# Kernel optimization log

Measured on AMD Instinct MI355X. Metric: run time of the kernel, lower is better.

Reference implementation:

```python
import jax, jax.numpy as jnp
import numpy as np

B, S, D = 2, 4096, 1024

def setup_inputs() -> dict:
    key = jax.random.key(0)
    k1, k2 = jax.random.split(key)
    x = jax.random.normal(k1, (B, S, D), dtype=jnp.float32)
    W = jax.random.normal(k2, (D, 3 * D), dtype=jnp.float32) * (1.0 / np.sqrt(D))
    b = jnp.zeros((3 * D,), dtype=jnp.float32)
    return {"x": x, "W": W, "b": b}

def reference(x, W, b) -> jnp.ndarray:
    D_ = x.shape[-1]
    qkv = x @ W + b                       # [B, S, 3D]
    q, k, v = jnp.split(qkv, 3, axis=2)    # each [B, S, D]
    scale = 1.0 / jnp.sqrt(jnp.asarray(D_, dtype=x.dtype))
    scores = jnp.einsum('bqd,bkd->bqk', q, k) * scale  # [B, S, S]
    weights = jax.nn.softmax(scores, axis=-1)
    return jnp.einsum('bqk,bkd->bqd', weights, v)       # [B, S, D]
```

## Files before the change

### kernel.cpp

```cpp
#include <hip/hip_runtime.h>
#include <hip/hip_bf16.h>

typedef __attribute__((ext_vector_type(4))) float  f32x4;
typedef __attribute__((ext_vector_type(8))) __bf16 bf16x8;
typedef __attribute__((ext_vector_type(8))) unsigned short u16x8;

typedef const __attribute__((address_space(1))) void gas_void;
typedef __attribute__((address_space(3))) void las_void;

__device__ __forceinline__ unsigned short f2bf(float x) {
    unsigned u = __builtin_bit_cast(unsigned, x);
    u += 0x7fffu + ((u >> 16) & 1u);
    return (unsigned short)(u >> 16);
}
__device__ __forceinline__ float bf2f(unsigned short h) {
    unsigned u = ((unsigned)h) << 16;
    return __builtin_bit_cast(float, u);
}
__device__ __forceinline__ void gload_lds16(const void* g, void* l) {
    __builtin_amdgcn_global_load_lds((gas_void*)g, (las_void*)l, 16, 0, 0);
}

#define WAITVM(N) asm volatile("s_waitcnt vmcnt(" #N ")" ::: "memory")
#define BAR() do { __builtin_amdgcn_s_barrier(); __builtin_amdgcn_sched_barrier(0); } while (0)

__global__ void k_f32_to_bf16(const float* __restrict__ in,
                              unsigned short* __restrict__ out, int n4) {
    int i = blockIdx.x * blockDim.x + threadIdx.x;
    if (i < n4) {
        float4 v = ((const float4*)in)[i];
        ushort4 o;
        o.x = f2bf(v.x); o.y = f2bf(v.y); o.z = f2bf(v.z); o.w = f2bf(v.w);
        ((ushort4*)out)[i] = o;
    }
}

__global__ void k_transpose_w(const float* __restrict__ W,
                              unsigned short* __restrict__ Wt,
                              int K, int N) {
    __shared__ unsigned short tile[32][33];
    int n0 = blockIdx.x * 32, k0 = blockIdx.y * 32;
    int tx = threadIdx.x, ty = threadIdx.y;
#pragma unroll
    for (int i = 0; i < 4; i++) {
        int kk = ty + i * 8;
        tile[kk][tx] = f2bf(W[(size_t)(k0 + kk) * N + n0 + tx]);
    }
    __syncthreads();
#pragma unroll
    for (int i = 0; i < 4; i++) {
        int nn = ty + i * 8;
        Wt[(size_t)(n0 + nn) * K + k0 + tx] = tile[tx][nn];
    }
}

__global__ __launch_bounds__(256, 2) void k_g128qkv(
        const unsigned short* __restrict__ A, int lda,
        const unsigned short* __restrict__ Bt, int ldb,
        unsigned short* __restrict__ C,
        unsigned short* __restrict__ Vt,
        const float* __restrict__ bias, int K) {
    __shared__ __align__(16) unsigned short As[2][8192];
    __shared__ __align__(16) unsigned short Bs[2][8192];

    const int nwg  = gridDim.x * gridDim.y;
    const int flat = blockIdx.y * gridDim.x + blockIdx.x;
    const int swzb = (flat & 7) * (nwg >> 3) + (flat >> 3);
    const int m0   = (swzb / gridDim.x) * 128;
    const int n0   = (swzb % gridDim.x) * 128;

    const int tid  = threadIdx.x;
    const int lane = tid & 63;
    const int wid  = tid >> 6;
    const int wr   = wid >> 1;
    const int wc   = wid & 1;
    const int l15  = lane & 15;
    const int l4   = lane >> 4;

    f32x4 acc[4][4] = {};

    const int srow = tid >> 3;
    const int kel  = (((lane & 7) ^ (lane >> 3)) << 3);
    const int c0 = (l4 << 4) ^ ((l15 & 7) << 4);
    const int c1 = (64 + (l4 << 4)) ^ ((l15 & 7) << 4);

    auto stA = [&](int b, int g, int kt) {
        gload_lds16(A + (size_t)(m0 + g * 32 + srow) * lda + kt * 64 + kel,
                    (char*)As + b * 16384 + g * 4096 + (wid << 10));
    };
    auto stB = [&](int b, int g, int kt) {
        gload_lds16(Bt + (size_t)(n0 + g * 32 + srow) * ldb + kt * 64 + kel,
                    (char*)Bs + b * 16384 + g * 4096 + (wid << 10));
    };

#define MM(I, J, X, Y) \
    acc[I][J] = __builtin_amdgcn_mfma_f32_16x16x32_bf16((X), (Y), acc[I][J], 0, 0, 0)

    const int NT = K >> 6;
    stA(0, 0, 0); stA(0, 1, 0); stA(0, 2, 0); stA(0, 3, 0);
    stB(0, 0, 0); stB(0, 1, 0); stB(0, 2, 0); stB(0, 3, 0);

    for (int t = 0; t < NT; t++) {
        const int cur = t & 1, nxt = cur ^ 1;
        const char* Ab = (const char*)As + cur * 16384;
        const char* Bb = (const char*)Bs + cur * 16384;
        const bool hn = (t + 1 < NT);

        bf16x8 af[4], bq[4];

        if (hn) {
            stA(nxt, 0, t + 1); stA(nxt, 1, t + 1); stA(nxt, 2, t + 1); stA(nxt, 3, t + 1);
            WAITVM(4);
        } else {
            WAITVM(0);
        }
        BAR();
#pragma unroll
        for (int mf = 0; mf < 4; mf++)
            af[mf] = *(const bf16x8*)(Ab + (wr * 64 + mf * 16 + l15) * 128 + c0);
#pragma unroll
        for (int nf = 0; nf < 4; nf++)
            bq[nf] = *(const bf16x8*)(Bb + (wc * 64 + nf * 16 + l15) * 128 + c0);
        __builtin_amdgcn_s_setprio(1);
#pragma unroll
        for (int mf = 0; mf < 4; mf++)
#pragma unroll
        for (int nf = 0; nf < 4; nf++)
            MM(mf, nf, af[mf], bq[nf]);
        __builtin_amdgcn_s_setprio(0);

        if (hn) {
            stB(nxt, 0, t + 1); stB(nxt, 1, t + 1); stB(nxt, 2, t + 1); stB(nxt, 3, t + 1);
        }
#pragma unroll
        for (int mf = 0; mf < 4; mf++)
            af[mf] = *(const bf16x8*)(Ab + (wr * 64 + mf * 16 + l15) * 128 + c1);
#pragma unroll
        for (int nf = 0; nf < 4; nf++)
            bq[nf] = *(const bf16x8*)(Bb + (wc * 64 + nf * 16 + l15) * 128 + c1);
        __builtin_amdgcn_s_setprio(1);
#pragma unroll
        for (int mf = 0; mf < 4; mf++)
#pragma unroll
        for (int nf = 0; nf < 4; nf++)
            MM(mf, nf, af[mf], bq[nf]);
        __builtin_amdgcn_s_setprio(0);
        BAR();
    }
#undef MM

#pragma unroll
    for (int mf = 0; mf < 4; mf++) {
        const int row = m0 + wr * 64 + mf * 16 + l4 * 4;
#pragma unroll
        for (int nf = 0; nf < 4; nf++) {
            const int col = n0 + wc * 64 + nf * 16 + l15;
            const f32x4 av = acc[mf][nf];
            const float bv = bias[col];
            const int lc = col & 1023;
            if (col < 2048) {
#pragma unroll
                for (int r = 0; r < 4; r++)
                    C[(size_t)(col >> 10) * 8388608 +
                      (size_t)(row + r) * 1024 + lc] = f2bf(av[r] + bv);
            } else {
                const int b = row >> 12, s = row & 4095;
                ushort4 o;
                o.x = f2bf(av[0] + bv); o.y = f2bf(av[1] + bv);
                o.z = f2bf(av[2] + bv); o.w = f2bf(av[3] + bv);
                *(ushort4*)&Vt[(size_t)b * 4194304 + (size_t)lc * 4096 + s] = o;
            }
        }
    }
}

__global__ __launch_bounds__(512, 2) void k_scores(
        const unsigned short* __restrict__ A,
        const unsigned short* __restrict__ Bt,
        unsigned short* __restrict__ C,
        float* __restrict__ part,
        int K, float scale, long sA, long sB, long sC) {
    __shared__ __align__(16) unsigned short As[2][16384];
    __shared__ __align__(16) unsigned short Bs[2][16384];

    const int z = blockIdx.z;
    A  += (size_t)z * sA;
    Bt += (size_t)z * sB;

    const int flat = blockIdx.y * gridDim.x + blockIdx.x;
    const int xcd  = flat & 7;
    const int i    = flat >> 3;
    const int m0   = (((xcd >> 1) << 2) + (i >> 3)) * 256;
    const int n0   = (((xcd & 1) << 3) + (i & 7)) * 256;

    const int tid  = threadIdx.x;
    const int lane = tid & 63;
    const int wid  = tid >> 6;
    const int wm   = wid >> 2;
    const int wn   = wid & 3;
    const int l15  = lane & 15;
    const int l4   = lane >> 4;

    f32x4 acc[8][4] = {};

    const int srow = tid >> 3;
    const int kel  = (((lane & 7) ^ (lane >> 3)) << 3);
    const int c0 = ((l4 << 4)) ^ ((l15 & 7) << 4);
    const int c1 = (64 + (l4 << 4)) ^ ((l15 & 7) << 4);

    auto stageA = [&](int b, int h, int kt) {
#pragma unroll
        for (int c = 0; c < 2; c++) {
            const int r = h * 128 + c * 64 + srow;
            gload_lds16(A + (size_t)(m0 + r) * 1024 + kt * 64 + kel,
                        (char*)As + b * 32768 + h * 16384 + c * 8192 + (wid << 10));
        }
    };
    auto stageB = [&](int b, int h, int kt) {
#pragma unroll
        for (int c = 0; c < 2; c++) {
            const int r = h * 128 + c * 64 + srow;
            gload_lds16(Bt + (size_t)(n0 + r) * 1024 + kt * 64 + kel,
                        (char*)Bs + b * 32768 + h * 16384 + c * 8192 + (wid << 10));
        }
    };

#define MM(I, J, X, Y) \
    acc[I][J] = __builtin_amdgcn_mfma_f32_16x16x32_bf16((X), (Y), acc[I][J], 0, 0, 0)

    const int NT = K >> 6;
    stageA(0, 0, 0); stageB(0, 0, 0); stageA(0, 1, 0); stageB(0, 1, 0);

    for (int t = 0; t < NT; t++) {
        const int cur = t & 1, nxt = cur ^ 1;
        const char* Ab = (const char*)As + cur * 32768;
        const char* Bb = (const char*)Bs + cur * 32768;

        if (t + 1 < NT) {
            stageA(nxt, 0, t + 1); stageB(nxt, 0, t + 1);
            stageA(nxt, 1, t + 1); stageB(nxt, 1, t + 1);
            WAITVM(8);
        } else {
            WAITVM(0);
        }
        BAR();

        bf16x8 bfrg[2][2][2];
#pragma unroll
        for (int qn = 0; qn < 2; qn++)
#pragma unroll
        for (int nf = 0; nf < 2; nf++) {
            const int rb = (wn * 64 + qn * 32 + nf * 16 + l15) * 128;
            bfrg[qn][nf][0] = *(const bf16x8*)(Bb + rb + c0);
            bfrg[qn][nf][1] = *(const bf16x8*)(Bb + rb + c1);
        }
        {
            bf16x8 af[4][2];
#pragma unroll
            for (int mf = 0; mf < 4; mf++) {
                const int ra = (wm * 128 + 0 * 64 + mf * 16 + l15) * 128;
                af[mf][0] = *(const bf16x8*)(Ab + ra + c0);
                af[mf][1] = *(const bf16x8*)(Ab + ra + c1);
            }
            __builtin_amdgcn_s_setprio(1);
#pragma unroll
            for (int mf = 0; mf < 4; mf++)
#pragma unroll
            for (int qn = 0; qn < 2; qn++)
#pragma unroll
            for (int nf = 0; nf < 2; nf++) {
                MM(mf, qn * 2 + nf, af[mf][0], bfrg[qn][nf][0]);
                MM(mf, qn * 2 + nf, af[mf][1], bfrg[qn][nf][1]);
            }
            __builtin_amdgcn_s_setprio(0);
        }

        {
            bf16x8 af[4][2];
#pragma unroll
            for (int mf = 0; mf < 4; mf++) {
                const int ra = (wm * 128 + 1 * 64 + mf * 16 + l15) * 128;
                af[mf][0] = *(const bf16x8*)(Ab + ra + c0);
                af[mf][1] = *(const bf16x8*)(Ab + ra + c1);
            }
            __builtin_amdgcn_s_setprio(1);
#pragma unroll
            for (int mf = 0; mf < 4; mf++)
#pragma unroll
            for (int qn = 0; qn < 2; qn++)
#pragma unroll
            for (int nf = 0; nf < 2; nf++) {
                MM(4 + mf, qn * 2 + nf, af[mf][0], bfrg[qn][nf][0]);
                MM(4 + mf, qn * 2 + nf, af[mf][1], bfrg[qn][nf][1]);
            }
            __builtin_amdgcn_s_setprio(0);
        }
        __builtin_amdgcn_s_barrier();
        __builtin_amdgcn_sched_barrier(0);
    }
#undef MM

    const int cb4 = ((n0 >> 8) << 2) + wn;
#pragma unroll
    for (int qm = 0; qm < 2; qm++)
#pragma unroll
    for (int mf = 0; mf < 4; mf++) {
        const int row = m0 + wm * 128 + qm * 64 + mf * 16 + l4 * 4;
        float rs[4] = {0.f, 0.f, 0.f, 0.f};
#pragma unroll
        for (int qn = 0; qn < 2; qn++)
#pragma unroll
        for (int nf = 0; nf < 2; nf++) {
            const int col = n0 + wn * 64 + qn * 32 + nf * 16 + l15;
            const f32x4 av = acc[qm * 4 + mf][qn * 2 + nf];
#pragma unroll
            for (int r = 0; r < 4; r++) {
                const float e = __expf(av[r] * scale);
                rs[r] += e;
                C[(size_t)z * sC + (size_t)(row + r) * 4096 + col] = f2bf(e);
            }
        }
#pragma unroll
        for (int r = 0; r < 4; r++) {
#pragma unroll
            for (int o = 1; o < 16; o <<= 1)
                rs[r] += __shfl_xor(rs[r], o);
        }
        if (l15 == 0) {
#pragma unroll
            for (int r = 0; r < 4; r++)
                part[((size_t)z * 4096 + row + r) * 64 + cb4] = rs[r];
        }
    }
}

__global__ __launch_bounds__(256) void k_rinv(const float* __restrict__ part,
                                              float* __restrict__ rinv, int nrows) {
    int row = blockIdx.x * blockDim.x + threadIdx.x;
    if (row < nrows) {
        const float* p = part + (size_t)row * 64;
        float s = 0.f;
#pragma unroll
        for (int i = 0; i < 16; i++) {
            f32x4 v = *(const f32x4*)(p + i * 4);
            s += v[0] + v[1] + v[2] + v[3];
        }
        rinv[row] = 1.0f / s;
    }
}

__global__ __launch_bounds__(512, 2) void k_pv256(
        const unsigned short* __restrict__ A,
        const unsigned short* __restrict__ Bt,
        float* __restrict__ C,
        const float* __restrict__ rinv,
        int K, long sA, long sB, long sC) {
    __shared__ __align__(16) unsigned short As[3][16384];
    __shared__ __align__(16) unsigned short Bs[3][8192];

    const int z = blockIdx.z;
    A  += (size_t)z * sA;
    Bt += (size_t)z * sB;

    const int nwg  = gridDim.x * gridDim.y;
    const int flat = blockIdx.y * gridDim.x + blockIdx.x;
    const int swzb = (flat & 7) * (nwg >> 3) + (flat >> 3);
    const int m0   = (swzb / gridDim.x) * 256;
    const int n0   = (swzb % gridDim.x) * 128;

    const int tid  = threadIdx.x;
    const int lane = tid & 63;
    const int wid  = tid >> 6;
    const int wm   = wid >> 2;
    const int wn   = wid & 3;
    const int l15  = lane & 15;
    const int l4   = lane >> 4;

    f32x4 acc[8][2] = {};

    const int srow = tid >> 3;
    const int kel  = (((lane & 7) ^ (lane >> 3)) << 3);
    const int c0 = ((l4 << 4)) ^ ((l15 & 7) << 4);
    const int c1 = (64 + (l4 << 4)) ^ ((l15 & 7) << 4);

    auto stageA1 = [&](int b, int a, int kt) {
        const int r = a * 64 + srow;
        gload_lds16(A + (size_t)(m0 + r) * 4096 + kt * 64 + kel,
                    (char*)As + b * 32768 + a * 8192 + (wid << 10));
    };
    auto stageB1 = [&](int b, int c, int kt) {
        const int r = c * 64 + srow;
        gload_lds16(Bt + (size_t)(n0 + r) * 4096 + kt * 64 + kel,
                    (char*)Bs + b * 16384 + c * 8192 + (wid << 10));
    };
    auto stageTile = [&](int b, int kt) {
        stageA1(b, 0, kt); stageA1(b, 1, kt);
        stageA1(b, 2, kt); stageA1(b, 3, kt);
        stageB1(b, 0, kt); stageB1(b, 1, kt);
    };

#define MM(I, J, X, Y) \
    acc[I][J] = __builtin_amdgcn_mfma_f32_16x16x32_bf16((X), (Y), acc[I][J], 0, 0, 0)

    const int NT = K >> 6;
    stageTile(0, 0);
    stageTile(1, 1);

    for (int t = 0; t < NT; t++) {
        const int cur = t % 3;
        const char* Ab = (const char*)As + cur * 32768;
        const char* Bb = (const char*)Bs + cur * 16384;

        if (t + 2 < NT) {
            stageTile((t + 2) % 3, t + 2);
            WAITVM(12);
        } else if (t + 1 < NT) {
            WAITVM(6);
        } else {
            WAITVM(0);
        }
        BAR();

        bf16x8 bfrg[2][2];
#pragma unroll
        for (int nf = 0; nf < 2; nf++) {
            const int rb = (wn * 32 + nf * 16 + l15) * 128;
            bfrg[nf][0] = *(const bf16x8*)(Bb + rb + c0);
            bfrg[nf][1] = *(const bf16x8*)(Bb + rb + c1);
        }
        {
            bf16x8 af[4][2];
#pragma unroll
            for (int mf = 0; mf < 4; mf++) {
                const int ra = (wm * 128 + 0 * 64 + mf * 16 + l15) * 128;
                af[mf][0] = *(const bf16x8*)(Ab + ra + c0);
                af[mf][1] = *(const bf16x8*)(Ab + ra + c1);
            }
            __builtin_amdgcn_s_setprio(1);
#pragma unroll
            for (int mf = 0; mf < 4; mf++)
#pragma unroll
            for (int nf = 0; nf < 2; nf++) {
                MM(mf, nf, af[mf][0], bfrg[nf][0]);
                MM(mf, nf, af[mf][1], bfrg[nf][1]);
            }
            __builtin_amdgcn_s_setprio(0);
        }

        {
            bf16x8 af[4][2];
#pragma unroll
            for (int mf = 0; mf < 4; mf++) {
                const int ra = (wm * 128 + 1 * 64 + mf * 16 + l15) * 128;
                af[mf][0] = *(const bf16x8*)(Ab + ra + c0);
                af[mf][1] = *(const bf16x8*)(Ab + ra + c1);
            }
            __builtin_amdgcn_s_setprio(1);
#pragma unroll
            for (int mf = 0; mf < 4; mf++)
#pragma unroll
            for (int nf = 0; nf < 2; nf++) {
                MM(4 + mf, nf, af[mf][0], bfrg[nf][0]);
                MM(4 + mf, nf, af[mf][1], bfrg[nf][1]);
            }
            __builtin_amdgcn_s_setprio(0);
        }
        __builtin_amdgcn_s_barrier();
        __builtin_amdgcn_sched_barrier(0);
    }
#undef MM

#pragma unroll
    for (int qm = 0; qm < 2; qm++)
#pragma unroll
    for (int mf = 0; mf < 4; mf++) {
        const int row = m0 + wm * 128 + qm * 64 + mf * 16 + l4 * 4;
        const f32x4 riv = *(const f32x4*)&rinv[(size_t)z * 4096 + row];
#pragma unroll
        for (int nf = 0; nf < 2; nf++) {
            const int col = n0 + wn * 32 + nf * 16 + l15;
            const f32x4 av = acc[qm * 4 + mf][nf];
#pragma unroll
            for (int r = 0; r < 4; r++)
                C[(size_t)z * sC + (size_t)(row + r) * 1024 + col] = av[r] * riv[r];
        }
    }
}

extern "C" void kernel_launch(void* const* d_in, const int* in_sizes, int n_in,
                              void* d_out, int out_size, void* d_ws, size_t ws_size,
                              hipStream_t stream) {
    const float* x    = (const float*)d_in[0];
    const float* W    = (const float*)d_in[1];
    const float* bias = (const float*)d_in[2];
    float* out        = (float*)d_out;

    char* ws = (char*)d_ws;
    unsigned short* Qb   = (unsigned short*)(ws);
    unsigned short* Vt   = (unsigned short*)(ws + 33554432);
    unsigned short* xb   = (unsigned short*)(ws + 50331648);
    unsigned short* Wt   = (unsigned short*)(ws + 67108864);
    unsigned short* Pcat = (unsigned short*)(ws + 50331648);
    float*          part = (float*)(ws + 117440512);
    float*          rinv = (float*)(ws + 121634816);

    k_f32_to_bf16<<<8192, 256, 0, stream>>>(x, xb, (8192 * 1024) / 4);
    k_transpose_w<<<dim3(96, 32), dim3(32, 8), 0, stream>>>(W, Wt, 1024, 3072);
    k_g128qkv<<<dim3(24, 64), 256, 0, stream>>>(xb, 1024, Wt, 1024, Qb, Vt, bias, 1024);

    const float scale = 0.03125f;
    k_scores<<<dim3(16, 16, 2), 512, 0, stream>>>(
        Qb, Qb + 8388608, Pcat, part, 1024, scale, 4194304, 4194304, 16777216);
    k_rinv<<<32, 256, 0, stream>>>(part, rinv, 8192);
    k_pv256<<<dim3(8, 16, 2), 512, 0, stream>>>(
        Pcat, Vt, out, rinv, 4096, 16777216, 4194304, 4194304);
}
```

Before: 258.8 us.

## Replace 256x256 scores GEMM with 128x128 tiles and split A/B staging

Swaps the scores kernel from 256x256 tiles with 512 threads and K-step 64 for 128x128 tiles with 256 threads and K-step 32, launching 2048 blocks instead of 512. The grid gets an XCD-aware swizzle, the LDS swizzle is adjusted, and B-tile prefetch moves after the MFMA block so A and B loads are spread across the iteration. The aim is better occupancy and load balance on the 256 CUs, at the cost of less operand reuse per tile, more global traffic, and more barriers per unit of work. Partial row sums still fit in 64 slots per row.

```diff
diff --git a/kernel.cpp b/kernel.cpp
--- a/kernel.cpp
+++ b/kernel.cpp
@@ -174,145 +174,97 @@
     }
 }
 
-__global__ __launch_bounds__(512, 2) void k_scores(
+__global__ __launch_bounds__(256, 2) void k_s128(
         const unsigned short* __restrict__ A,
         const unsigned short* __restrict__ Bt,
         unsigned short* __restrict__ C,
         float* __restrict__ part,
         int K, float scale, long sA, long sB, long sC) {
-    __shared__ __align__(16) unsigned short As[2][16384];
-    __shared__ __align__(16) unsigned short Bs[2][16384];
+    __shared__ __align__(16) unsigned short As[2][4096];
+    __shared__ __align__(16) unsigned short Bs[2][4096];
 
     const int z = blockIdx.z;
     A  += (size_t)z * sA;
     Bt += (size_t)z * sB;
 
+    const int nwg  = gridDim.x * gridDim.y;
     const int flat = blockIdx.y * gridDim.x + blockIdx.x;
-    const int xcd  = flat & 7;
-    const int i    = flat >> 3;
-    const int m0   = (((xcd >> 1) << 2) + (i >> 3)) * 256;
-    const int n0   = (((xcd & 1) << 3) + (i & 7)) * 256;
+    const int swzb = (flat & 7) * (nwg >> 3) + (flat >> 3);
+    const int m0   = (swzb / gridDim.x) * 128;
+    const int n0   = (swzb % gridDim.x) * 128;
 
     const int tid  = threadIdx.x;
     const int lane = tid & 63;
     const int wid  = tid >> 6;
-    const int wm   = wid >> 2;
-    const int wn   = wid & 3;
+    const int wr   = wid >> 1;
+    const int wc   = wid & 1;
     const int l15  = lane & 15;
     const int l4   = lane >> 4;
 
-    f32x4 acc[8][4] = {};
-
-    const int srow = tid >> 3;
-    const int kel  = (((lane & 7) ^ (lane >> 3)) << 3);
-    const int c0 = ((l4 << 4)) ^ ((l15 & 7) << 4);
-    const int c1 = (64 + (l4 << 4)) ^ ((l15 & 7) << 4);
-
-    auto stageA = [&](int b, int h, int kt) {
-#pragma unroll
-        for (int c = 0; c < 2; c++) {
-            const int r = h * 128 + c * 64 + srow;
-            gload_lds16(A + (size_t)(m0 + r) * 1024 + kt * 64 + kel,
-                        (char*)As + b * 32768 + h * 16384 + c * 8192 + (wid << 10));
-        }
-    };
-    auto stageB = [&](int b, int h, int kt) {
-#pragma unroll
-        for (int c = 0; c < 2; c++) {
-            const int r = h * 128 + c * 64 + srow;
-            gload_lds16(Bt + (size_t)(n0 + r) * 1024 + kt * 64 + kel,
-                        (char*)Bs + b * 32768 + h * 16384 + c * 8192 + (wid << 10));
-        }
+    f32x4 acc[4][4] = {};
+
+    const int srow = tid >> 2;
+    const int kel  = (((tid & 3) ^ ((tid >> 2) & 3)) << 3);
+    const int csw  = ((l4 ^ (l15 & 3)) << 4);
+
+    auto stA = [&](int b, int g, int kt) {
+        gload_lds16(A + (size_t)(m0 + g * 64 + srow) * 1024 + kt * 32 + kel,
+                    (char*)As + b * 8192 + g * 4096 + (wid << 10));
+    };
+    auto stB = [&](int b, int g, int kt) {
+        gload_lds16(Bt + (size_t)(n0 + g * 64 + srow) * 1024 + kt * 32 + kel,
+                    (char*)Bs + b * 8192 + g * 4096 + (wid << 10));
     };
 
 #define MM(I, J, X, Y) \
     acc[I][J] = __builtin_amdgcn_mfma_f32_16x16x32_bf16((X), (Y), acc[I][J], 0, 0, 0)
 
-    const int NT = K >> 6;
-    stageA(0, 0, 0); stageB(0, 0, 0); stageA(0, 1, 0); stageB(0, 1, 0);
+    const int NT = K >> 5;
+    stA(0, 0, 0); stA(0, 1, 0); stB(0, 0, 0); stB(0, 1, 0);
 
     for (int t = 0; t < NT; t++) {
         const int cur = t & 1, nxt = cur ^ 1;
-        const char* Ab = (const char*)As + cur * 32768;
-        const char* Bb = (const char*)Bs + cur * 32768;
-
-        if (t + 1 < NT) {
-            stageA(nxt, 0, t + 1); stageB(nxt, 0, t + 1);
-            stageA(nxt, 1, t + 1); stageB(nxt, 1, t + 1);
-            WAITVM(8);
+        const char* Ab = (const char*)As + cur * 8192;
+        const char* Bb = (const char*)Bs + cur * 8192;
+        const bool hn = (t + 1 < NT);
+
+        if (hn) {
+            stA(nxt, 0, t + 1); stA(nxt, 1, t + 1);
+            WAITVM(2);
         } else {
             WAITVM(0);
         }
         BAR();
 
-        bf16x8 bfrg[2][2][2];
-#pragma unroll
-        for (int qn = 0; qn < 2; qn++)
-#pragma unroll
-        for (int nf = 0; nf < 2; nf++) {
-            const int rb = (wn * 64 + qn * 32 + nf * 16 + l15) * 128;
-            bfrg[qn][nf][0] = *(const bf16x8*)(Bb + rb + c0);
-            bfrg[qn][nf][1] = *(const bf16x8*)(Bb + rb + c1);
-        }
-        {
-            bf16x8 af[4][2];
-#pragma unroll
-            for (int mf = 0; mf < 4; mf++) {
-                const int ra = (wm * 128 + 0 * 64 + mf * 16 + l15) * 128;
-                af[mf][0] = *(const bf16x8*)(Ab + ra + c0);
-                af[mf][1] = *(const bf16x8*)(Ab + ra + c1);
-            }
-            __builtin_amdgcn_s_setprio(1);
-#pragma unroll
-            for (int mf = 0; mf < 4; mf++)
-#pragma unroll
-            for (int qn = 0; qn < 2; qn++)
-#pragma unroll
-            for (int nf = 0; nf < 2; nf++) {
-                MM(mf, qn * 2 + nf, af[mf][0], bfrg[qn][nf][0]);
-                MM(mf, qn * 2 + nf, af[mf][1], bfrg[qn][nf][1]);
-            }
-            __builtin_amdgcn_s_setprio(0);
-        }
-
-        {
-            bf16x8 af[4][2];
-#pragma unroll
-            for (int mf = 0; mf < 4; mf++) {
-                const int ra = (wm * 128 + 1 * 64 + mf * 16 + l15) * 128;
-                af[mf][0] = *(const bf16x8*)(Ab + ra + c0);
-                af[mf][1] = *(const bf16x8*)(Ab + ra + c1);
-            }
-            __builtin_amdgcn_s_setprio(1);
-#pragma unroll
-            for (int mf = 0; mf < 4; mf++)
-#pragma unroll
-            for (int qn = 0; qn < 2; qn++)
-#pragma unroll
-            for (int nf = 0; nf < 2; nf++) {
-                MM(4 + mf, qn * 2 + nf, af[mf][0], bfrg[qn][nf][0]);
-                MM(4 + mf, qn * 2 + nf, af[mf][1], bfrg[qn][nf][1]);
-            }
-            __builtin_amdgcn_s_setprio(0);
-        }
-        __builtin_amdgcn_s_barrier();
-        __builtin_amdgcn_sched_barrier(0);
+        bf16x8 af[4], bq[4];
+#pragma unroll
+        for (int mf = 0; mf < 4; mf++)
+            af[mf] = *(const bf16x8*)(Ab + (wr * 64 + mf * 16 + l15) * 64 + csw);
+#pragma unroll
+        for (int nf = 0; nf < 4; nf++)
+            bq[nf] = *(const bf16x8*)(Bb + (wc * 64 + nf * 16 + l15) * 64 + csw);
+        __builtin_amdgcn_s_setprio(1);
+#pragma unroll
+        for (int mf = 0; mf < 4; mf++)
+#pragma unroll
+        for (int nf = 0; nf < 4; nf++)
+            MM(mf, nf, af[mf], bq[nf]);
+        __builtin_amdgcn_s_setprio(0);
+
+        if (hn) { stB(nxt, 0, t + 1); stB(nxt, 1, t + 1); }
+        BAR();
     }
 #undef MM
 
-    const int cb4 = ((n0 >> 8) << 2) + wn;
-#pragma unroll
-    for (int qm = 0; qm < 2; qm++)
+    const int slot = ((n0 >> 7) << 1) + wc;
 #pragma unroll
     for (int mf = 0; mf < 4; mf++) {
-        const int row = m0 + wm * 128 + qm * 64 + mf * 16 + l4 * 4;
+        const int row = m0 + wr * 64 + mf * 16 + l4 * 4;
         float rs[4] = {0.f, 0.f, 0.f, 0.f};
 #pragma unroll
-        for (int qn = 0; qn < 2; qn++)
-#pragma unroll
-        for (int nf = 0; nf < 2; nf++) {
-            const int col = n0 + wn * 64 + qn * 32 + nf * 16 + l15;
-            const f32x4 av = acc[qm * 4 + mf][qn * 2 + nf];
+        for (int nf = 0; nf < 4; nf++) {
+            const int col = n0 + wc * 64 + nf * 16 + l15;
+            const f32x4 av = acc[mf][nf];
 #pragma unroll
             for (int r = 0; r < 4; r++) {
                 const float e = __expf(av[r] * scale);
@@ -329,7 +281,7 @@
         if (l15 == 0) {
 #pragma unroll
             for (int r = 0; r < 4; r++)
-                part[((size_t)z * 4096 + row + r) * 64 + cb4] = rs[r];
+                part[((size_t)z * 4096 + row + r) * 64 + slot] = rs[r];
         }
     }
 }
@@ -446,7 +398,6 @@
             }
             __builtin_amdgcn_s_setprio(0);
         }
-
         {
             bf16x8 af[4][2];
 #pragma unroll
@@ -509,7 +460,7 @@
     k_g128qkv<<<dim3(24, 64), 256, 0, stream>>>(xb, 1024, Wt, 1024, Qb, Vt, bias, 1024);
 
     const float scale = 0.03125f;
-    k_scores<<<dim3(16, 16, 2), 512, 0, stream>>>(
+    k_s128<<<dim3(32, 32, 2), 256, 0, stream>>>(
         Qb, Qb + 8388608, Pcat, part, 1024, scale, 4194304, 4194304, 16777216);
     k_rinv<<<32, 256, 0, stream>>>(part, rinv, 8192);
     k_pv256<<<dim3(8, 16, 2), 512, 0, stream>>>(
```

Measured after the change: 267.7 us. +3.4%, slower.
